# Kernel optimization log

Measured on AMD Instinct MI355X. Metric: run time of the kernel, lower is better.

Reference implementation:

```python
import jax, jax.numpy as jnp
import numpy as np

N_HEADS = 16
D_MODEL = 2048
DK = D_MODEL // N_HEADS
SEQ = 2048


def setup_inputs() -> dict:
    key = jax.random.key(0)
    ks = jax.random.split(key, 11)
    s = 0.02
    return {
        "query": jax.random.normal(ks[0], (SEQ, D_MODEL), jnp.float32),
        "key": jax.random.normal(ks[1], (SEQ, D_MODEL), jnp.float32),
        "value": jax.random.normal(ks[2], (SEQ, D_MODEL), jnp.float32),
        # per-head projection weights, stacked over heads: [H, d_model, dk]
        "Wq": jax.random.normal(ks[3], (N_HEADS, D_MODEL, DK), jnp.float32) * s,
        "bq": jnp.zeros((N_HEADS, DK), jnp.float32),
        "Wk": jax.random.normal(ks[4], (N_HEADS, D_MODEL, DK), jnp.float32) * s,
        "bk": jnp.zeros((N_HEADS, DK), jnp.float32),
        "Wv": jax.random.normal(ks[5], (N_HEADS, D_MODEL, DK), jnp.float32) * s,
        "bv": jnp.zeros((N_HEADS, DK), jnp.float32),
        # output projection: [H*dk, d_model]
        "Wo": jax.random.normal(ks[6], (N_HEADS * DK, D_MODEL), jnp.float32) * s,
        "bo": jnp.zeros((D_MODEL,), jnp.float32),
    }


def reference(query, key, value, Wq, bq, Wk, bk, Wv, bv, Wo, bo):
    # Per-head linear projections, batched over heads. q/k/v: [H, S, dk]
    q = jnp.einsum('sd,hdk->hsk', query, Wq) + bq[:, None, :]
    k = jnp.einsum('sd,hdk->hsk', key, Wk) + bk[:, None, :]
    v = jnp.einsum('sd,hdk->hsk', value, Wv) + bv[:, None, :]
    scale = jnp.sqrt(jnp.asarray(DK, q.dtype))
    # scores: [H, S_q, S_k]
    scores = jnp.einsum('hsk,htk->hst', q, k) / scale
    # Faithful to original: Softmax(dim=0) on each 2D [S_q, S_k] matrix
    # -> normalize over the QUERY axis (axis=1 here).
    attn = jax.nn.softmax(scores, axis=1)
    heads = jnp.einsum('hst,htk->hsk', attn, v)  # [H, S, dk]
    # torch.cat(attentions, dim=1): [S, H*dk]
    concat = jnp.transpose(heads, (1, 0, 2)).reshape(SEQ, N_HEADS * DK)
    return concat @ Wo + bo
```

## Files before the change

kernel.cpp:

```cpp
#include <hip/hip_runtime.h>

#define SEQ 2048
#define DMODEL 2048
#define NHEADS 16
#define DKH 128

typedef __bf16 bf16;
typedef __attribute__((ext_vector_type(8))) __bf16 bf16x8;
typedef __attribute__((ext_vector_type(4))) __bf16 bf16x4;
typedef __attribute__((ext_vector_type(4))) float f32x4;

#define AS1 __attribute__((address_space(1)))
#define AS3 __attribute__((address_space(3)))

__device__ __forceinline__ void async_copy16(const void* g, void* l) {
  __builtin_amdgcn_global_load_lds((AS1 void*)(unsigned long long)g,
                                   (AS3 void*)l, 16, 0, 0);
}

__device__ __forceinline__ int swz(int chunk, int row) {
  return (chunk ^ (row & 7)) << 3;
}

template <typename OutT, bool BIAS>
__global__ __launch_bounds__(256) void gemm_bt(
    const bf16* __restrict__ A, const bf16* __restrict__ B,
    const float* __restrict__ bias, OutT* __restrict__ C,
    int M, int N, int K, int lda, int ldb, int ldo, float scale,
    long long sA, long long sB, long long sC, long long sBias) {
  A += (long long)blockIdx.z * sA;
  B += (long long)blockIdx.z * sB;
  C += (long long)blockIdx.z * sC;
  const float* biasp = BIAS ? (bias + (long long)blockIdx.z * sBias) : nullptr;

  const int m0 = blockIdx.y * 128;
  const int n0 = blockIdx.x * 128;

  __shared__ __align__(16) bf16 As[128 * 64];
  __shared__ __align__(16) bf16 Bs[128 * 64];

  const int tid = threadIdx.x;
  const int wave = tid >> 6;
  const int lane = tid & 63;
  const int srow = wave * 8 + (lane >> 3);
  const int scol = ((lane & 7) ^ (lane >> 3)) * 8;
  const int wr = (wave >> 1) * 64;
  const int wc = (wave & 1) * 64;
  const int lr = lane & 15;
  const int quad = lane >> 4;

  const bf16* ag = A + (long long)(m0 + srow) * lda + scol;
  const bf16* bg = B + (long long)(n0 + srow) * ldb + scol;

  f32x4 acc[4][4];
#pragma unroll
  for (int i = 0; i < 4; ++i)
#pragma unroll
    for (int j = 0; j < 4; ++j) {
      acc[i][j][0] = 0.f; acc[i][j][1] = 0.f;
      acc[i][j][2] = 0.f; acc[i][j][3] = 0.f;
    }

  for (int kt = 0; kt < K; kt += 64) {
#pragma unroll
    for (int i = 0; i < 4; ++i) {
      async_copy16(ag + kt + (long long)i * 32 * lda, As + (i * 32 + wave * 8) * 64);
      async_copy16(bg + kt + (long long)i * 32 * ldb, Bs + (i * 32 + wave * 8) * 64);
    }
    __syncthreads();
#pragma unroll
    for (int kk = 0; kk < 64; kk += 32) {
      bf16x8 af[4], bfr[4];
#pragma unroll
      for (int i = 0; i < 4; ++i) {
        const int ra = wr + i * 16 + lr;
        const int rb = wc + i * 16 + lr;
        af[i]  = *(const bf16x8*)(As + ra * 64 + swz((kk >> 3) + quad, ra));
        bfr[i] = *(const bf16x8*)(Bs + rb * 64 + swz((kk >> 3) + quad, rb));
      }
#pragma unroll
      for (int i = 0; i < 4; ++i)
#pragma unroll
        for (int j = 0; j < 4; ++j)
          acc[i][j] = __builtin_amdgcn_mfma_f32_16x16x32_bf16(af[i], bfr[j], acc[i][j], 0, 0, 0);
    }
    __syncthreads();
  }

#pragma unroll
  for (int j = 0; j < 4; ++j) {
    const int n = n0 + wc + j * 16 + lr;
    const float bv = BIAS ? biasp[n] : 0.f;
#pragma unroll
    for (int i = 0; i < 4; ++i) {
      const int mb = m0 + wr + i * 16 + quad * 4;
#pragma unroll
      for (int r = 0; r < 4; ++r)
        C[(long long)(mb + r) * ldo + n] = (OutT)(acc[i][j][r] * scale + bv);
    }
  }
}

__global__ __launch_bounds__(256) void qk_exp(
    const bf16* __restrict__ q, const bf16* __restrict__ k,
    bf16* __restrict__ E, float* __restrict__ lpart) {
  const int h = blockIdx.z;
  const bf16* A = q + h * DKH;
  const bf16* B = k + h * DKH;
  bf16* C = E + (long long)h * SEQ * SEQ;

  const int m0 = blockIdx.y * 128;
  const int n0 = blockIdx.x * 128;

  __shared__ __align__(16) bf16 As[128 * 64];
  __shared__ __align__(16) bf16 Bs[128 * 64];

  const int tid = threadIdx.x;
  const int wave = tid >> 6;
  const int lane = tid & 63;
  const int srow = wave * 8 + (lane >> 3);
  const int scol = ((lane & 7) ^ (lane >> 3)) * 8;
  const int wr = (wave >> 1) * 64;
  const int wc = (wave & 1) * 64;
  const int lr = lane & 15;
  const int quad = lane >> 4;

  const bf16* ag = A + (long long)(m0 + srow) * DMODEL + scol;
  const bf16* bg = B + (long long)(n0 + srow) * DMODEL + scol;

  f32x4 acc[4][4];
#pragma unroll
  for (int i = 0; i < 4; ++i)
#pragma unroll
    for (int j = 0; j < 4; ++j) {
      acc[i][j][0] = 0.f; acc[i][j][1] = 0.f;
      acc[i][j][2] = 0.f; acc[i][j][3] = 0.f;
    }

  for (int kt = 0; kt < DKH; kt += 64) {
#pragma unroll
    for (int i = 0; i < 4; ++i) {
      async_copy16(ag + kt + (long long)i * 32 * DMODEL, As + (i * 32 + wave * 8) * 64);
      async_copy16(bg + kt + (long long)i * 32 * DMODEL, Bs + (i * 32 + wave * 8) * 64);
    }
    __syncthreads();
#pragma unroll
    for (int kk = 0; kk < 64; kk += 32) {
      bf16x8 af[4], bfr[4];
#pragma unroll
      for (int i = 0; i < 4; ++i) {
        const int ra = wr + i * 16 + lr;
        const int rb = wc + i * 16 + lr;
        af[i]  = *(const bf16x8*)(As + ra * 64 + swz((kk >> 3) + quad, ra));
        bfr[i] = *(const bf16x8*)(Bs + rb * 64 + swz((kk >> 3) + quad, rb));
      }
#pragma unroll
      for (int i = 0; i < 4; ++i)
#pragma unroll
        for (int j = 0; j < 4; ++j)
          acc[i][j] = __builtin_amdgcn_mfma_f32_16x16x32_bf16(af[i], bfr[j], acc[i][j], 0, 0, 0);
    }
    __syncthreads();
  }

  const float scale = 0.08838834764831845f;
  float* sml = (float*)As;

#pragma unroll
  for (int j = 0; j < 4; ++j) {
    const int n = n0 + wc + j * 16 + lr;
    float l_loc = 0.f;
#pragma unroll
    for (int i = 0; i < 4; ++i) {
      const int mb = m0 + wr + i * 16 + quad * 4;
#pragma unroll
      for (int r = 0; r < 4; ++r) {
        bf16 ev = (bf16)__expf(acc[i][j][r] * scale);
        C[(long long)(mb + r) * SEQ + n] = ev;
        l_loc += (float)ev;
      }
    }
    l_loc += __shfl_xor(l_loc, 16, 64);
    l_loc += __shfl_xor(l_loc, 32, 64);
    if (quad == 0)
      sml[(wave >> 1) * 128 + wc + j * 16 + lr] = l_loc;
  }
  __syncthreads();
  if (tid < 128)
    lpart[((long long)h * 16 + blockIdx.y) * SEQ + n0 + tid] =
        sml[tid] + sml[128 + tid];
}

__global__ void sm_sum(const float* __restrict__ lp, float* __restrict__ rvec) {
  const int i = blockIdx.x * 256 + threadIdx.x;
  const int h = i >> 11, t = i & (SEQ - 1);
  float l = 0.f;
#pragma unroll
  for (int rb = 0; rb < 16; ++rb)
    l += lp[((long long)h * 16 + rb) * SEQ + t];
  rvec[i] = 1.f / l;
}

__global__ void vscale(bf16* __restrict__ vt, const float* __restrict__ rvec) {
  const int cg = blockIdx.y;
  const int t0 = threadIdx.x * 8;
  const float* r = rvec + (cg >> 7) * SEQ;
  bf16x8 v = *(const bf16x8*)(vt + (long long)cg * SEQ + t0);
#pragma unroll
  for (int e = 0; e < 8; ++e) v[e] = (bf16)((float)v[e] * r[t0 + e]);
  *(bf16x8*)(vt + (long long)cg * SEQ + t0) = v;
}

__global__ __launch_bounds__(256) void pv_gemm(
    const bf16* __restrict__ Sc, const bf16* __restrict__ VT,
    bf16* __restrict__ O) {
  const int h = blockIdx.y;
  const int m0 = blockIdx.x * 64;
  const bf16* A = Sc + (long long)h * SEQ * SEQ;
  const bf16* B = VT + (long long)h * DKH * SEQ;

  __shared__ __align__(16) bf16 As[64 * 64];
  __shared__ __align__(16) bf16 Bs[128 * 64];

  const int tid = threadIdx.x;
  const int wave = tid >> 6;
  const int lane = tid & 63;
  const int srow = wave * 8 + (lane >> 3);
  const int scol = ((lane & 7) ^ (lane >> 3)) * 8;
  const int wr = (wave >> 1) * 32;
  const int wc = (wave & 1) * 64;
  const int lr = lane & 15;
  const int quad = lane >> 4;

  const bf16* ag = A + (long long)(m0 + srow) * SEQ + scol;
  const bf16* bg = B + (long long)srow * SEQ + scol;

  f32x4 acc[2][4];
#pragma unroll
  for (int i = 0; i < 2; ++i)
#pragma unroll
    for (int j = 0; j < 4; ++j) {
      acc[i][j][0] = 0.f; acc[i][j][1] = 0.f;
      acc[i][j][2] = 0.f; acc[i][j][3] = 0.f;
    }

  for (int kt = 0; kt < SEQ; kt += 64) {
#pragma unroll
    for (int i = 0; i < 2; ++i)
      async_copy16(ag + kt + (long long)i * 32 * SEQ, As + (i * 32 + wave * 8) * 64);
#pragma unroll
    for (int i = 0; i < 4; ++i)
      async_copy16(bg + kt + (long long)i * 32 * SEQ, Bs + (i * 32 + wave * 8) * 64);
    __syncthreads();
#pragma unroll
    for (int kk = 0; kk < 64; kk += 32) {
      bf16x8 af[2], bfr[4];
#pragma unroll
      for (int i = 0; i < 2; ++i) {
        const int ra = wr + i * 16 + lr;
        af[i] = *(const bf16x8*)(As + ra * 64 + swz((kk >> 3) + quad, ra));
      }
#pragma unroll
      for (int j = 0; j < 4; ++j) {
        const int rb = wc + j * 16 + lr;
        bfr[j] = *(const bf16x8*)(Bs + rb * 64 + swz((kk >> 3) + quad, rb));
      }
#pragma unroll
      for (int i = 0; i < 2; ++i)
#pragma unroll
        for (int j = 0; j < 4; ++j)
          acc[i][j] = __builtin_amdgcn_mfma_f32_16x16x32_bf16(af[i], bfr[j], acc[i][j], 0, 0, 0);
    }
    __syncthreads();
  }

#pragma unroll
  for (int j = 0; j < 4; ++j) {
    const int c = h * DKH + wc + j * 16 + lr;
#pragma unroll
    for (int i = 0; i < 2; ++i) {
      const int mb = m0 + wr + i * 16 + quad * 4;
#pragma unroll
      for (int r = 0; r < 4; ++r)
        O[(long long)(mb + r) * DMODEL + c] = (bf16)acc[i][j][r];
    }
  }
}

__global__ void cvt3_f32_to_bf16(const float* __restrict__ a, const float* __restrict__ b,
                                 const float* __restrict__ c, bf16* __restrict__ out,
                                 long long n) {
  const float* src = blockIdx.z == 0 ? a : (blockIdx.z == 1 ? b : c);
  long long i = ((long long)blockIdx.x * blockDim.x + threadIdx.x) * 4;
  if (i >= n) return;
  const float4 v = *(const float4*)(src + i);
  bf16x4 o;
  o[0] = (bf16)v.x; o[1] = (bf16)v.y; o[2] = (bf16)v.z; o[3] = (bf16)v.w;
  *(bf16x4*)(out + blockIdx.z * n + i) = o;
}

__global__ void transposeW3(const float* __restrict__ Wq, const float* __restrict__ Wk,
                            const float* __restrict__ Wv, bf16* __restrict__ out) {
  __shared__ float tile[32][33];
  const int z = blockIdx.z;
  const int g = z >> 4, hh = z & 15;
  const float* in = (g == 0 ? Wq : (g == 1 ? Wk : Wv)) + (long long)hh * DMODEL * DKH;
  bf16* o = out + (long long)z * DMODEL * DKH;
  const int c0 = blockIdx.x * 32, r0 = blockIdx.y * 32;
  const int tx = threadIdx.x, ty = threadIdx.y;
#pragma unroll
  for (int j = 0; j < 32; j += 8)
    tile[ty + j][tx] = in[(long long)(r0 + ty + j) * DKH + c0 + tx];
  __syncthreads();
#pragma unroll
  for (int j = 0; j < 32; j += 8)
    o[(long long)(c0 + ty + j) * DMODEL + r0 + tx] = (bf16)tile[tx][ty + j];
}

template <typename T>
__global__ void transpose_to_bf16(const T* __restrict__ in, bf16* __restrict__ out,
                                  int R, int Cc) {
  __shared__ float tile[32][33];
  const int c0 = blockIdx.x * 32, r0 = blockIdx.y * 32;
  const int tx = threadIdx.x, ty = threadIdx.y;
#pragma unroll
  for (int j = 0; j < 32; j += 8)
    tile[ty + j][tx] = (float)in[(long long)(r0 + ty + j) * Cc + c0 + tx];
  __syncthreads();
#pragma unroll
  for (int j = 0; j < 32; j += 8)
    out[(long long)(c0 + ty + j) * R + r0 + tx] = (bf16)tile[tx][ty + j];
}

__global__ void pack_bias3(const float* __restrict__ a, const float* __restrict__ b,
                           const float* __restrict__ c, float* __restrict__ o) {
  int i = blockIdx.x * 256 + threadIdx.x;
  if (i < NHEADS * DKH) {
    o[i] = a[i];
    o[NHEADS * DKH + i] = b[i];
    o[2 * NHEADS * DKH + i] = c[i];
  }
}

extern "C" void kernel_launch(void* const* d_in, const int* in_sizes, int n_in,
                              void* d_out, int out_size, void* d_ws, size_t ws_size,
                              hipStream_t stream) {
  const float* query = (const float*)d_in[0];
  const float* key_  = (const float*)d_in[1];
  const float* value = (const float*)d_in[2];
  const float* Wq = (const float*)d_in[3];
  const float* bq = (const float*)d_in[4];
  const float* Wk = (const float*)d_in[5];
  const float* bk = (const float*)d_in[6];
  const float* Wv = (const float*)d_in[7];
  const float* bv = (const float*)d_in[8];
  const float* Wo = (const float*)d_in[9];
  const float* bo = (const float*)d_in[10];
  float* out = (float*)d_out;

  const long long elems = (long long)SEQ * DMODEL;
  const long long SZB = elems * 2;

  char* ws = (char*)d_ws;
  bf16* Qb = (bf16*)ws;
  bf16* Wt = (bf16*)(ws + 3 * SZB);
  bf16* scores = (bf16*)ws;
  char* p = ws + (long long)NHEADS * SEQ * SEQ * 2;
  float* biasQKV = (float*)p; p += 32 * 1024;
  bf16* Wot   = (bf16*)p; p += SZB;
  bf16* qkv   = (bf16*)p; p += 3 * SZB;
  bf16* vt    = (bf16*)p; p += SZB;
  bf16* heads = (bf16*)p; p += SZB;
  float* lpart = (float*)p; p += (long long)NHEADS * 16 * SEQ * 4;
  float* rvec  = (float*)p; p += (long long)NHEADS * SEQ * 4;
  if ((size_t)(p - ws) > ws_size) return;

  cvt3_f32_to_bf16<<<dim3(elems / 1024, 1, 3), 256, 0, stream>>>(query, key_, value, Qb, elems);
  transposeW3<<<dim3(DKH / 32, DMODEL / 32, 48), dim3(32, 8), 0, stream>>>(Wq, Wk, Wv, Wt);
  transpose_to_bf16<float><<<dim3(DMODEL / 32, DMODEL / 32), dim3(32, 8), 0, stream>>>(Wo, Wot, DMODEL, DMODEL);
  pack_bias3<<<(NHEADS * DKH + 255) / 256, 256, 0, stream>>>(bq, bk, bv, biasQKV);

  gemm_bt<bf16, true><<<dim3(16, 16, 3), 256, 0, stream>>>(
      Qb, Wt, biasQKV, qkv, SEQ, DMODEL, DMODEL, DMODEL, DMODEL, DMODEL, 1.f,
      elems, elems, elems, (long long)DMODEL);

  transpose_to_bf16<bf16><<<dim3(DMODEL / 32, SEQ / 32), dim3(32, 8), 0, stream>>>(
      qkv + 2 * elems, vt, SEQ, DMODEL);

  qk_exp<<<dim3(16, 16, NHEADS), 256, 0, stream>>>(qkv, qkv + elems, scores, lpart);

  sm_sum<<<NHEADS * SEQ / 256, 256, 0, stream>>>(lpart, rvec);

  vscale<<<dim3(1, DMODEL), 256, 0, stream>>>(vt, rvec);

  pv_gemm<<<dim3(SEQ / 64, NHEADS), 256, 0, stream>>>(scores, vt, heads);

  gemm_bt<float, true><<<dim3(16, 16, 1), 256, 0, stream>>>(
      heads, Wot, bo, out, SEQ, DMODEL, DMODEL, DMODEL, DMODEL, DMODEL, 1.f, 0, 0, 0, 0);
}
```

Baseline: 359.6 us.

## Reuse Q tile across key strips in qk_exp and split-K output projection

qk_exp now loads the full 128-wide Q tile once and loops over four 128-column key tiles per block. This cuts redundant Q loads and block count, and the partial row-sum output is widened to 32 entries. The output projection is split along K into two batched GEMMs writing fp32 partials, followed by a reduce kernel that adds bias. The split is meant to raise occupancy on the 256-block final GEMM, at the cost of extra fp32 traffic and one more launch.

```diff
diff --git a/kernel.cpp b/kernel.cpp
--- a/kernel.cpp
+++ b/kernel.cpp
@@ -20,6 +20,9 @@
 
 __device__ __forceinline__ int swz(int chunk, int row) {
   return (chunk ^ (row & 7)) << 3;
+}
+__device__ __forceinline__ int swz16(int chunk, int row) {
+  return (chunk ^ (row & 15)) << 3;
 }
 
 template <typename OutT, bool BIAS>
@@ -105,54 +108,62 @@
     const bf16* __restrict__ q, const bf16* __restrict__ k,
     bf16* __restrict__ E, float* __restrict__ lpart) {
   const int h = blockIdx.z;
-  const bf16* A = q + h * DKH;
-  const bf16* B = k + h * DKH;
+  const int m0 = blockIdx.y * 128;
+  const int nstrip = blockIdx.x * 512;
+  const bf16* A = q + (long long)h * DKH;
+  const bf16* B = k + (long long)h * DKH;
   bf16* C = E + (long long)h * SEQ * SEQ;
 
-  const int m0 = blockIdx.y * 128;
-  const int n0 = blockIdx.x * 128;
-
-  __shared__ __align__(16) bf16 As[128 * 64];
-  __shared__ __align__(16) bf16 Bs[128 * 64];
+  __shared__ __align__(16) bf16 As[128 * 128];
+  __shared__ __align__(16) bf16 Bs[128 * 128];
 
   const int tid = threadIdx.x;
   const int wave = tid >> 6;
   const int lane = tid & 63;
-  const int srow = wave * 8 + (lane >> 3);
-  const int scol = ((lane & 7) ^ (lane >> 3)) * 8;
   const int wr = (wave >> 1) * 64;
   const int wc = (wave & 1) * 64;
   const int lr = lane & 15;
   const int quad = lane >> 4;
-
-  const bf16* ag = A + (long long)(m0 + srow) * DMODEL + scol;
-  const bf16* bg = B + (long long)(n0 + srow) * DMODEL + scol;
-
-  f32x4 acc[4][4];
-#pragma unroll
-  for (int i = 0; i < 4; ++i)
-#pragma unroll
-    for (int j = 0; j < 4; ++j) {
-      acc[i][j][0] = 0.f; acc[i][j][1] = 0.f;
-      acc[i][j][2] = 0.f; acc[i][j][3] = 0.f;
-    }
-
-  for (int kt = 0; kt < DKH; kt += 64) {
-#pragma unroll
-    for (int i = 0; i < 4; ++i) {
-      async_copy16(ag + kt + (long long)i * 32 * DMODEL, As + (i * 32 + wave * 8) * 64);
-      async_copy16(bg + kt + (long long)i * 32 * DMODEL, Bs + (i * 32 + wave * 8) * 64);
+  const float scale = 0.08838834764831845f;
+
+  for (int nt = 0; nt < 4; ++nt) {
+    if (nt) __syncthreads();
+#pragma unroll
+    for (int it = 0; it < 8; ++it) {
+      const int row = wave * 32 + it * 4 + (lane >> 4);
+      const int chunk = (lane & 15) ^ (row & 15);
+      async_copy16(B + (long long)(nstrip + nt * 128 + row) * DMODEL + chunk * 8,
+                   Bs + (wave * 32 + it * 4) * 128);
+    }
+    if (nt == 0) {
+#pragma unroll
+      for (int it = 0; it < 8; ++it) {
+        const int row = wave * 32 + it * 4 + (lane >> 4);
+        const int chunk = (lane & 15) ^ (row & 15);
+        async_copy16(A + (long long)(m0 + row) * DMODEL + chunk * 8,
+                     As + (wave * 32 + it * 4) * 128);
+      }
     }
     __syncthreads();
-#pragma unroll
-    for (int kk = 0; kk < 64; kk += 32) {
+
+    f32x4 acc[4][4];
+#pragma unroll
+    for (int i = 0; i < 4; ++i)
+#pragma unroll
+      for (int j = 0; j < 4; ++j) {
+        acc[i][j][0] = 0.f; acc[i][j][1] = 0.f;
+        acc[i][j][2] = 0.f; acc[i][j][3] = 0.f;
+      }
+
+#pragma unroll
+    for (int kk = 0; kk < 128; kk += 32) {
       bf16x8 af[4], bfr[4];
 #pragma unroll
       for (int i = 0; i < 4; ++i) {
         const int ra = wr + i * 16 + lr;
         const int rb = wc + i * 16 + lr;
-        af[i]  = *(const bf16x8*)(As + ra * 64 + swz((kk >> 3) + quad, ra));
-        bfr[i] = *(const bf16x8*)(Bs + rb * 64 + swz((kk >> 3) + quad, rb));
+        af[i]  = *(const bf16x8*)(As + ra * 128 + swz16((kk >> 3) + quad, ra));
+        bfr[i] = *(const bf16x8*)(Bs + rb * 128 + swz16((kk >> 3) + quad, rb));
       }
 #pragma unroll
       for (int i = 0; i < 4; ++i)
@@ -160,35 +171,27 @@
         for (int j = 0; j < 4; ++j)
           acc[i][j] = __builtin_amdgcn_mfma_f32_16x16x32_bf16(af[i], bfr[j], acc[i][j], 0, 0, 0);
     }
-    __syncthreads();
-  }
-
-  const float scale = 0.08838834764831845f;
-  float* sml = (float*)As;
-
-#pragma unroll
-  for (int j = 0; j < 4; ++j) {
-    const int n = n0 + wc + j * 16 + lr;
-    float l_loc = 0.f;
-#pragma unroll
-    for (int i = 0; i < 4; ++i) {
-      const int mb = m0 + wr + i * 16 + quad * 4;
-#pragma unroll
-      for (int r = 0; r < 4; ++r) {
-        bf16 ev = (bf16)__expf(acc[i][j][r] * scale);
-        C[(long long)(mb + r) * SEQ + n] = ev;
-        l_loc += (float)ev;
-      }
-    }
-    l_loc += __shfl_xor(l_loc, 16, 64);
-    l_loc += __shfl_xor(l_loc, 32, 64);
-    if (quad == 0)
-      sml[(wave >> 1) * 128 + wc + j * 16 + lr] = l_loc;
-  }
-  __syncthreads();
-  if (tid < 128)
-    lpart[((long long)h * 16 + blockIdx.y) * SEQ + n0 + tid] =
-        sml[tid] + sml[128 + tid];
+
+#pragma unroll
+    for (int j = 0; j < 4; ++j) {
+      const int n = nstrip + nt * 128 + wc + j * 16 + lr;
+      float l_loc = 0.f;
+#pragma unroll
+      for (int i = 0; i < 4; ++i) {
+        const int mb = m0 + wr + i * 16 + quad * 4;
+#pragma unroll
+        for (int r = 0; r < 4; ++r) {
+          bf16 ev = (bf16)__expf(acc[i][j][r] * scale);
+          C[(long long)(mb + r) * SEQ + n] = ev;
+          l_loc += (float)ev;
+        }
+      }
+      l_loc += __shfl_xor(l_loc, 16, 64);
+      l_loc += __shfl_xor(l_loc, 32, 64);
+      if (quad == 0)
+        lpart[((long long)h * 32 + blockIdx.y * 2 + (wave >> 1)) * SEQ + n] = l_loc;
+    }
+  }
 }
 
 __global__ void sm_sum(const float* __restrict__ lp, float* __restrict__ rvec) {
@@ -196,8 +199,8 @@
   const int h = i >> 11, t = i & (SEQ - 1);
   float l = 0.f;
 #pragma unroll
-  for (int rb = 0; rb < 16; ++rb)
-    l += lp[((long long)h * 16 + rb) * SEQ + t];
+  for (int rb = 0; rb < 32; ++rb)
+    l += lp[((long long)h * 32 + rb) * SEQ + t];
   rvec[i] = 1.f / l;
 }
 
@@ -285,6 +288,18 @@
         O[(long long)(mb + r) * DMODEL + c] = (bf16)acc[i][j][r];
     }
   }
+}
+
+__global__ void reduce_bias(const float* __restrict__ p, const float* __restrict__ bo,
+                            float* __restrict__ out) {
+  const long long i = ((long long)blockIdx.x * 256 + threadIdx.x) * 4;
+  const float4 a = *(const float4*)(p + i);
+  const float4 b = *(const float4*)(p + (long long)SEQ * DMODEL + i);
+  const float4 bb = *(const float4*)(bo + (i & (DMODEL - 1)));
+  float4 o;
+  o.x = a.x + b.x + bb.x; o.y = a.y + b.y + bb.y;
+  o.z = a.z + b.z + bb.z; o.w = a.w + b.w + bb.w;
+  *(float4*)(out + i) = o;
 }
 
 __global__ void cvt3_f32_to_bf16(const float* __restrict__ a, const float* __restrict__ b,
@@ -365,13 +380,14 @@
   bf16* Qb = (bf16*)ws;
   bf16* Wt = (bf16*)(ws + 3 * SZB);
   bf16* scores = (bf16*)ws;
+  float* Opart = (float*)ws;
   char* p = ws + (long long)NHEADS * SEQ * SEQ * 2;
   float* biasQKV = (float*)p; p += 32 * 1024;
   bf16* Wot   = (bf16*)p; p += SZB;
   bf16* qkv   = (bf16*)p; p += 3 * SZB;
   bf16* vt    = (bf16*)p; p += SZB;
   bf16* heads = (bf16*)p; p += SZB;
-  float* lpart = (float*)p; p += (long long)NHEADS * 16 * SEQ * 4;
+  float* lpart = (float*)p; p += (long long)NHEADS * 32 * SEQ * 4;
   float* rvec  = (float*)p; p += (long long)NHEADS * SEQ * 4;
   if ((size_t)(p - ws) > ws_size) return;
 
@@ -387,7 +403,7 @@
   transpose_to_bf16<bf16><<<dim3(DMODEL / 32, SEQ / 32), dim3(32, 8), 0, stream>>>(
       qkv + 2 * elems, vt, SEQ, DMODEL);
 
-  qk_exp<<<dim3(16, 16, NHEADS), 256, 0, stream>>>(qkv, qkv + elems, scores, lpart);
+  qk_exp<<<dim3(4, 16, NHEADS), 256, 0, stream>>>(qkv, qkv + elems, scores, lpart);
 
   sm_sum<<<NHEADS * SEQ / 256, 256, 0, stream>>>(lpart, rvec);
 
@@ -395,6 +411,9 @@
 
   pv_gemm<<<dim3(SEQ / 64, NHEADS), 256, 0, stream>>>(scores, vt, heads);
 
-  gemm_bt<float, true><<<dim3(16, 16, 1), 256, 0, stream>>>(
-      heads, Wot, bo, out, SEQ, DMODEL, DMODEL, DMODEL, DMODEL, DMODEL, 1.f, 0, 0, 0, 0);
-}
+  gemm_bt<float, false><<<dim3(16, 16, 2), 256, 0, stream>>>(
+      heads, Wot, nullptr, Opart, SEQ, DMODEL, 1024, DMODEL, DMODEL, DMODEL, 1.f,
+      1024, 1024, elems, 0);
+
+  reduce_bias<<<elems / 1024, 256, 0, stream>>>(Opart, bo, out);
+}
```

New measurement: 353.2 us. About the same (-1.8%).
